# Performance work log

Measured on AMD Instinct MI355X. Metric: run time of the kernel, lower is better.

Reference implementation:

```python
import jax, jax.numpy as jnp
import numpy as np

N_NODES = 100000
N_EDGES = 1000000
IN_DIM = 128
OUT_DIM = 64


def setup_inputs() -> dict:
    key = jax.random.key(0)
    k1, k2, k3, k4, k5 = jax.random.split(key, 5)
    X = jax.random.normal(k1, (N_NODES, IN_DIM), dtype=jnp.float32)
    edge_rows = jax.random.randint(k2, (N_EDGES,), 0, N_NODES, dtype=jnp.int64)
    edge_cols = jax.random.randint(k3, (N_EDGES,), 0, N_NODES, dtype=jnp.int64)
    # normalized adjacency values (e.g. 1/sqrt(d_i d_j)), positive and small
    edge_vals = jax.random.uniform(k4, (N_EDGES,), dtype=jnp.float32, minval=0.0, maxval=1.0)
    # xavier-uniform-ish weight
    limit = float(np.sqrt(6.0 / (IN_DIM + OUT_DIM)))
    W = jax.random.uniform(k5, (IN_DIM, OUT_DIM), dtype=jnp.float32, minval=-limit, maxval=limit)
    bias = jnp.zeros((OUT_DIM,), dtype=jnp.float32)
    return {"X": X, "edge_rows": edge_rows, "edge_cols": edge_cols,
            "edge_vals": edge_vals, "W": W, "bias": bias}


def reference(X, edge_rows, edge_cols, edge_vals, W, bias):
    # dense projection: (N, in_dim) @ (in_dim, out_dim) -> (N, out_dim)
    h = X @ W
    # spmm over COO sparse A_norm: out[r] += v * h[c] for each edge (r, c, v)
    msg = edge_vals[:, None] * h[edge_cols]          # (E, out_dim) gather
    agg = jax.ops.segment_sum(msg, edge_rows, num_segments=N_NODES)
    return jax.nn.relu(agg + bias)
```

## Files before the change

### kernel.cpp

```cpp
#include <hip/hip_runtime.h>

#define IN_DIM 128
#define OUT_DIM 64
#define RPB_SHIFT 6
#define RPB 64
#define NBMAX 2048
#define CHUNK 4096
#define SLABCAP 896
#define PADK 136

typedef __attribute__((ext_vector_type(8))) short bf16x8;
typedef __attribute__((ext_vector_type(4))) float f32x4;
typedef __attribute__((ext_vector_type(4))) unsigned short us4;

__device__ inline unsigned short f2bf(float f) {
  unsigned u = __float_as_uint(f);
  u += 0x7FFFu + ((u >> 16) & 1u);
  return (unsigned short)(u >> 16);
}

__global__ __launch_bounds__(256) void zero_int_kernel(int* __restrict__ p, int n) {
  int i = blockIdx.x * 256 + threadIdx.x;
  for (; i < n; i += gridDim.x * 256) p[i] = 0;
}

__global__ __launch_bounds__(512) void fat_kernel(const float* __restrict__ X,
                                                  const float* __restrict__ W,
                                                  unsigned short* __restrict__ H,
                                                  const int* __restrict__ rows,
                                                  const int* __restrict__ cols,
                                                  const float* __restrict__ vals,
                                                  int* __restrict__ cursor,
                                                  uint2* __restrict__ staged,
                                                  int n, int ne, int nb, int nPart) {
  __shared__ __align__(16) unsigned char smem[34816];
  const int t = threadIdx.x;

  if ((int)blockIdx.x < nPart) {
    int* lh    = (int*)smem;
    int* lbase = (int*)(smem + NBMAX * 4);
    const int e0 = blockIdx.x * CHUNK;
    const int e1 = min(e0 + CHUNK, ne);

    for (int i = t; i < nb; i += 512) lh[i] = 0;
    __syncthreads();

    for (int i = e0 + t; i < e1; i += 512)
      atomicAdd(&lh[rows[i] >> RPB_SHIFT], 1);
    __syncthreads();

    for (int i = t; i < nb; i += 512) {
      int c = lh[i];
      lbase[i] = c ? atomicAdd(&cursor[i], c) : 0;
    }
    __syncthreads();
    for (int i = t; i < nb; i += 512) lh[i] = 0;
    __syncthreads();

    for (int i = e0 + t; i < e1; i += 512) {
      int r = rows[i];
      int b = r >> RPB_SHIFT;
      int lofs = atomicAdd(&lh[b], 1);
      int pos = lbase[b] + lofs;
      if (pos < SLABCAP) {
        unsigned key = ((unsigned)(r & (RPB - 1)) << 17) | (unsigned)cols[i];
        staged[(size_t)b * SLABCAP + pos] = make_uint2(key, __float_as_uint(vals[i]));
      }
    }
  } else {
    unsigned short (*Xs)[PADK] = (unsigned short(*)[PADK])smem;
    unsigned short (*Wt)[PADK] = (unsigned short(*)[PADK])(smem + 17408);
    const int lane = t & 63;
    const int wave = t >> 6;
    const int sub = wave & 3;
    const int ch = wave >> 2;
    const int row0 = ((int)blockIdx.x - nPart) * 64;

    {
      const float4* w4 = (const float4*)W;
#pragma unroll
      for (int j = 0; j < 4; ++j) {
        int i4 = t + j * 512;
        int k = i4 >> 4;
        int c = (i4 & 15) * 4;
        float4 v = w4[i4];
        Wt[c + 0][k] = f2bf(v.x);
        Wt[c + 1][k] = f2bf(v.y);
        Wt[c + 2][k] = f2bf(v.z);
        Wt[c + 3][k] = f2bf(v.w);
      }
    }
    {
#pragma unroll
      for (int j = 0; j < 4; ++j) {
        int i4 = t + j * 512;
        int r = i4 >> 5;
        int c4 = i4 & 31;
        int row = row0 + r;
        if (row < n) {
          float4 v = ((const float4*)(X + (size_t)row * IN_DIM))[c4];
          us4 p;
          p.x = f2bf(v.x); p.y = f2bf(v.y); p.z = f2bf(v.z); p.w = f2bf(v.w);
          *(us4*)&Xs[r][c4 * 4] = p;
        }
      }
    }
    __syncthreads();

    f32x4 acc[2] = {};
    const int arow = sub * 16 + (lane & 15);
    const int kg = (lane >> 4) * 8;
#pragma unroll
    for (int kk = 0; kk < 4; ++kk) {
      bf16x8 a = *(const bf16x8*)&Xs[arow][kk * 32 + kg];
#pragma unroll
      for (int nt = 0; nt < 2; ++nt) {
        bf16x8 b = *(const bf16x8*)&Wt[ch * 32 + nt * 16 + (lane & 15)][kk * 32 + kg];
        acc[nt] = __builtin_amdgcn_mfma_f32_16x16x32_bf16(a, b, acc[nt], 0, 0, 0);
      }
    }

    const int orow0 = row0 + sub * 16 + (lane >> 4) * 4;
#pragma unroll
    for (int nt = 0; nt < 2; ++nt) {
      int col = ch * 32 + nt * 16 + (lane & 15);
#pragma unroll
      for (int r = 0; r < 4; ++r) {
        int row = orow0 + r;
        if (row < n) H[(size_t)row * OUT_DIM + col] = f2bf(acc[nt][r]);
      }
    }
  }
}

__global__ __launch_bounds__(512) void spmm_fused_kernel(const int* __restrict__ cursor,
                                                         const uint2* __restrict__ staged,
                                                         const unsigned short* __restrict__ H,
                                                         const float* __restrict__ bias,
                                                         float* __restrict__ out, int n) {
  __shared__ uint2 sorted[SLABCAP];
  __shared__ int rcnt[RPB];
  __shared__ int rstart[RPB];
  __shared__ int rcur[RPB];

  const int b = blockIdx.x;
  const int t = threadIdx.x;
  const int cnt = min(cursor[b], SLABCAP);
  const uint2* slab = staged + (size_t)b * SLABCAP;

  if (t < RPB) rcnt[t] = 0;
  __syncthreads();
  for (int i = t; i < cnt; i += 512) atomicAdd(&rcnt[slab[i].x >> 17], 1);
  __syncthreads();

  if (t < RPB) {
    int v = rcnt[t];
    int x = v;
#pragma unroll
    for (int d = 1; d < RPB; d <<= 1) {
      int y = __shfl_up(x, d);
      if (t >= d) x += y;
    }
    rstart[t] = x - v;
    rcur[t] = x - v;
  }
  __syncthreads();

  for (int i = t; i < cnt; i += 512) {
    uint2 e = slab[i];
    int rl = e.x >> 17;
    int pos = atomicAdd(&rcur[rl], 1);
    sorted[pos] = e;
  }
  __syncthreads();

  const int lane = t & 63;
  const int wave = t >> 6;
  const int q4 = (lane & 15) * 4;
  const float4 bv = *(const float4*)&bias[q4];
  const int row0 = b << RPB_SHIFT;

  for (int rl = wave * 4 + ((lane >> 4) & 3); rl < RPB; rl += 32) {
    const int s = rstart[rl];
    const int c = rcnt[rl];
    float a0 = 0.f, a1 = 0.f, a2 = 0.f, a3 = 0.f;
    int e = 0;
    for (; e + 4 <= c; e += 4) {
      float v[4];
      uint2 hu[4];
#pragma unroll
      for (int k = 0; k < 4; ++k) {
        uint2 en = sorted[s + e + k];
        hu[k] = *(const uint2*)&H[(size_t)(en.x & 0x1FFFF) * OUT_DIM + q4];
        v[k] = __uint_as_float(en.y);
      }
#pragma unroll
      for (int k = 0; k < 4; ++k) {
        a0 = fmaf(v[k], __uint_as_float(hu[k].x << 16), a0);
        a1 = fmaf(v[k], __uint_as_float(hu[k].x & 0xFFFF0000u), a1);
        a2 = fmaf(v[k], __uint_as_float(hu[k].y << 16), a2);
        a3 = fmaf(v[k], __uint_as_float(hu[k].y & 0xFFFF0000u), a3);
      }
    }
    for (; e < c; ++e) {
      uint2 en = sorted[s + e];
      uint2 hu = *(const uint2*)&H[(size_t)(en.x & 0x1FFFF) * OUT_DIM + q4];
      float v = __uint_as_float(en.y);
      a0 = fmaf(v, __uint_as_float(hu.x << 16), a0);
      a1 = fmaf(v, __uint_as_float(hu.x & 0xFFFF0000u), a1);
      a2 = fmaf(v, __uint_as_float(hu.y << 16), a2);
      a3 = fmaf(v, __uint_as_float(hu.y & 0xFFFF0000u), a3);
    }
    int row = row0 + rl;
    if (row < n) {
      float4 o;
      o.x = fmaxf(a0 + bv.x, 0.f);
      o.y = fmaxf(a1 + bv.y, 0.f);
      o.z = fmaxf(a2 + bv.z, 0.f);
      o.w = fmaxf(a3 + bv.w, 0.f);
      *(float4*)(out + (size_t)row * OUT_DIM + q4) = o;
    }
  }
}

extern "C" void kernel_launch(void* const* d_in, const int* in_sizes, int n_in,
                              void* d_out, int out_size, void* d_ws, size_t ws_size,
                              hipStream_t stream) {
  const float* X    = (const float*)d_in[0];
  const int*   rows = (const int*)d_in[1];
  const int*   cols = (const int*)d_in[2];
  const float* vals = (const float*)d_in[3];
  const float* W    = (const float*)d_in[4];
  const float* bias = (const float*)d_in[5];
  float* out = (float*)d_out;

  const int n_nodes = in_sizes[0] / IN_DIM;
  const int n_edges = in_sizes[1];
  const int nb = (n_nodes + RPB - 1) >> RPB_SHIFT;

  char* ws = (char*)d_ws;
  unsigned short* H = (unsigned short*)ws;
  size_t off = (size_t)n_nodes * OUT_DIM * sizeof(unsigned short);
  off = (off + 15) & ~(size_t)15;
  int* cursor  = (int*)(ws + off); off += NBMAX * 4;
  uint2* staged = (uint2*)(ws + off);

  const int nPart = (n_edges + CHUNK - 1) / CHUNK;
  const int nGemm = (n_nodes + 63) / 64;

  zero_int_kernel<<<8, 256, 0, stream>>>(cursor, nb);
  fat_kernel<<<nPart + nGemm, 512, 0, stream>>>(X, W, H, rows, cols, vals, cursor, staged,
                                                n_nodes, n_edges, nb, nPart);
  spmm_fused_kernel<<<nb, 512, 0, stream>>>(cursor, staged, H, bias, out, n_nodes);
}
```

Measured before the change: 64.24 us.

## Split fused kernel into prep, GEMM, and sub-slab atomic scatter kernels

Replaces the combined partition/GEMM kernel with three kernels. A prep kernel zeroes the cursors and pre-transposes W to bf16. The GEMM kernel reads X directly from global memory, with no LDS staging, and computes all 64 columns per wave. Edge bucketing now uses direct global atomics on eight sub-slabs per row block, keyed by block index, instead of per-block LDS histograms. This removes the two-pass histogram and reduces atomic contention, but it adds launches, serializes the GEMM and the scatter, and spreads capacity across fixed-size sub-slabs that could overflow.

```diff
diff --git a/kernel.cpp b/kernel.cpp
--- a/kernel.cpp
+++ b/kernel.cpp
@@ -4,10 +4,8 @@
 #define OUT_DIM 64
 #define RPB_SHIFT 6
 #define RPB 64
-#define NBMAX 2048
-#define CHUNK 4096
+#define SUBCAP 176
 #define SLABCAP 896
-#define PADK 136
 
 typedef __attribute__((ext_vector_type(8))) short bf16x8;
 typedef __attribute__((ext_vector_type(4))) float f32x4;
@@ -19,116 +17,79 @@
   return (unsigned short)(u >> 16);
 }
 
-__global__ __launch_bounds__(256) void zero_int_kernel(int* __restrict__ p, int n) {
-  int i = blockIdx.x * 256 + threadIdx.x;
-  for (; i < n; i += gridDim.x * 256) p[i] = 0;
-}
-
-__global__ __launch_bounds__(512) void fat_kernel(const float* __restrict__ X,
-                                                  const float* __restrict__ W,
-                                                  unsigned short* __restrict__ H,
-                                                  const int* __restrict__ rows,
-                                                  const int* __restrict__ cols,
-                                                  const float* __restrict__ vals,
-                                                  int* __restrict__ cursor,
-                                                  uint2* __restrict__ staged,
-                                                  int n, int ne, int nb, int nPart) {
-  __shared__ __align__(16) unsigned char smem[34816];
+__global__ __launch_bounds__(256) void prep_kernel(const float* __restrict__ W,
+                                                   unsigned short* __restrict__ WT,
+                                                   int* __restrict__ cursor, int ncur) {
+  const int bid = blockIdx.x, t = threadIdx.x;
+  if (bid < 8) {
+    for (int i = bid * 256 + t; i < ncur; i += 8 * 256) cursor[i] = 0;
+  } else {
+    int gid = (bid - 8) * 256 + t;
+    int c = gid >> 5;
+    int kb = (gid & 31) * 4;
+    us4 p;
+    p.x = f2bf(W[(kb + 0) * OUT_DIM + c]);
+    p.y = f2bf(W[(kb + 1) * OUT_DIM + c]);
+    p.z = f2bf(W[(kb + 2) * OUT_DIM + c]);
+    p.w = f2bf(W[(kb + 3) * OUT_DIM + c]);
+    *(us4*)(WT + c * IN_DIM + kb) = p;
+  }
+}
+
+__global__ __launch_bounds__(256) void gemm_kernel(const float* __restrict__ X,
+                                                   const unsigned short* __restrict__ WT,
+                                                   unsigned short* __restrict__ H, int n) {
   const int t = threadIdx.x;
-
-  if ((int)blockIdx.x < nPart) {
-    int* lh    = (int*)smem;
-    int* lbase = (int*)(smem + NBMAX * 4);
-    const int e0 = blockIdx.x * CHUNK;
-    const int e1 = min(e0 + CHUNK, ne);
-
-    for (int i = t; i < nb; i += 512) lh[i] = 0;
-    __syncthreads();
-
-    for (int i = e0 + t; i < e1; i += 512)
-      atomicAdd(&lh[rows[i] >> RPB_SHIFT], 1);
-    __syncthreads();
-
-    for (int i = t; i < nb; i += 512) {
-      int c = lh[i];
-      lbase[i] = c ? atomicAdd(&cursor[i], c) : 0;
-    }
-    __syncthreads();
-    for (int i = t; i < nb; i += 512) lh[i] = 0;
-    __syncthreads();
-
-    for (int i = e0 + t; i < e1; i += 512) {
-      int r = rows[i];
-      int b = r >> RPB_SHIFT;
-      int lofs = atomicAdd(&lh[b], 1);
-      int pos = lbase[b] + lofs;
-      if (pos < SLABCAP) {
-        unsigned key = ((unsigned)(r & (RPB - 1)) << 17) | (unsigned)cols[i];
-        staged[(size_t)b * SLABCAP + pos] = make_uint2(key, __float_as_uint(vals[i]));
-      }
-    }
-  } else {
-    unsigned short (*Xs)[PADK] = (unsigned short(*)[PADK])smem;
-    unsigned short (*Wt)[PADK] = (unsigned short(*)[PADK])(smem + 17408);
-    const int lane = t & 63;
-    const int wave = t >> 6;
-    const int sub = wave & 3;
-    const int ch = wave >> 2;
-    const int row0 = ((int)blockIdx.x - nPart) * 64;
-
-    {
-      const float4* w4 = (const float4*)W;
-#pragma unroll
-      for (int j = 0; j < 4; ++j) {
-        int i4 = t + j * 512;
-        int k = i4 >> 4;
-        int c = (i4 & 15) * 4;
-        float4 v = w4[i4];
-        Wt[c + 0][k] = f2bf(v.x);
-        Wt[c + 1][k] = f2bf(v.y);
-        Wt[c + 2][k] = f2bf(v.z);
-        Wt[c + 3][k] = f2bf(v.w);
-      }
-    }
-    {
-#pragma unroll
-      for (int j = 0; j < 4; ++j) {
-        int i4 = t + j * 512;
-        int r = i4 >> 5;
-        int c4 = i4 & 31;
-        int row = row0 + r;
-        if (row < n) {
-          float4 v = ((const float4*)(X + (size_t)row * IN_DIM))[c4];
-          us4 p;
-          p.x = f2bf(v.x); p.y = f2bf(v.y); p.z = f2bf(v.z); p.w = f2bf(v.w);
-          *(us4*)&Xs[r][c4 * 4] = p;
-        }
-      }
-    }
-    __syncthreads();
-
-    f32x4 acc[2] = {};
-    const int arow = sub * 16 + (lane & 15);
-    const int kg = (lane >> 4) * 8;
-#pragma unroll
-    for (int kk = 0; kk < 4; ++kk) {
-      bf16x8 a = *(const bf16x8*)&Xs[arow][kk * 32 + kg];
-#pragma unroll
-      for (int nt = 0; nt < 2; ++nt) {
-        bf16x8 b = *(const bf16x8*)&Wt[ch * 32 + nt * 16 + (lane & 15)][kk * 32 + kg];
-        acc[nt] = __builtin_amdgcn_mfma_f32_16x16x32_bf16(a, b, acc[nt], 0, 0, 0);
-      }
-    }
-
-    const int orow0 = row0 + sub * 16 + (lane >> 4) * 4;
-#pragma unroll
-    for (int nt = 0; nt < 2; ++nt) {
-      int col = ch * 32 + nt * 16 + (lane & 15);
-#pragma unroll
-      for (int r = 0; r < 4; ++r) {
-        int row = orow0 + r;
-        if (row < n) H[(size_t)row * OUT_DIM + col] = f2bf(acc[nt][r]);
-      }
+  const int lane = t & 63;
+  const int sub = t >> 6;
+  const int row0 = blockIdx.x * 64;
+  const int r16 = lane & 15;
+  const int kg = (lane >> 4) * 8;
+  const int rowA = min(row0 + sub * 16 + r16, n - 1);
+  const float* xr = X + (size_t)rowA * IN_DIM + kg;
+
+  f32x4 acc[4] = {};
+#pragma unroll
+  for (int kk = 0; kk < 4; ++kk) {
+    float4 u = *(const float4*)(xr + kk * 32);
+    float4 v = *(const float4*)(xr + kk * 32 + 4);
+    bf16x8 a;
+    a[0] = (short)f2bf(u.x); a[1] = (short)f2bf(u.y);
+    a[2] = (short)f2bf(u.z); a[3] = (short)f2bf(u.w);
+    a[4] = (short)f2bf(v.x); a[5] = (short)f2bf(v.y);
+    a[6] = (short)f2bf(v.z); a[7] = (short)f2bf(v.w);
+#pragma unroll
+    for (int ct = 0; ct < 4; ++ct) {
+      bf16x8 b = *(const bf16x8*)(WT + (ct * 16 + r16) * IN_DIM + kk * 32 + kg);
+      acc[ct] = __builtin_amdgcn_mfma_f32_16x16x32_bf16(a, b, acc[ct], 0, 0, 0);
+    }
+  }
+
+  const int orow0 = row0 + sub * 16 + (lane >> 4) * 4;
+#pragma unroll
+  for (int ct = 0; ct < 4; ++ct) {
+    int col = ct * 16 + r16;
+#pragma unroll
+    for (int r = 0; r < 4; ++r) {
+      int row = orow0 + r;
+      if (row < n) H[(size_t)row * OUT_DIM + col] = f2bf(acc[ct][r]);
+    }
+  }
+}
+
+__global__ __launch_bounds__(256) void scatter_kernel(const int* __restrict__ rows,
+                                                      const int* __restrict__ cols,
+                                                      const float* __restrict__ vals,
+                                                      int* __restrict__ cursor,
+                                                      uint2* __restrict__ staged, int ne) {
+  const int g = blockIdx.x & 7;
+  for (int i = blockIdx.x * 256 + threadIdx.x; i < ne; i += gridDim.x * 256) {
+    int r = rows[i];
+    int slot = ((r >> RPB_SHIFT) << 3) + g;
+    int pos = atomicAdd(&cursor[slot], 1);
+    if (pos < SUBCAP) {
+      unsigned key = ((unsigned)(r & (RPB - 1)) << 17) | (unsigned)cols[i];
+      staged[(size_t)slot * SUBCAP + pos] = make_uint2(key, __float_as_uint(vals[i]));
     }
   }
 }
@@ -142,15 +103,32 @@
   __shared__ int rcnt[RPB];
   __shared__ int rstart[RPB];
   __shared__ int rcur[RPB];
+  __shared__ int segc[8];
 
   const int b = blockIdx.x;
   const int t = threadIdx.x;
-  const int cnt = min(cursor[b], SLABCAP);
-  const uint2* slab = staged + (size_t)b * SLABCAP;
-
+  const int lane = t & 63;
+  const int wave = t >> 6;
+
+  if (t < 8) segc[t] = min(cursor[b * 8 + t], SUBCAP);
   if (t < RPB) rcnt[t] = 0;
   __syncthreads();
-  for (int i = t; i < cnt; i += 512) atomicAdd(&rcnt[slab[i].x >> 17], 1);
+  if (t == 0) {
+    int s = 0;
+    for (int j = 0; j < 8; ++j) {
+      int c = segc[j];
+      if (s + c > SLABCAP) c = SLABCAP - s;
+      segc[j] = c;
+      s += c;
+    }
+  }
+  __syncthreads();
+
+  {
+    const uint2* seg = staged + (size_t)(b * 8 + wave) * SUBCAP;
+    const int c = segc[wave];
+    for (int i = lane; i < c; i += 64) atomicAdd(&rcnt[seg[i].x >> 17], 1);
+  }
   __syncthreads();
 
   if (t < RPB) {
@@ -166,16 +144,17 @@
   }
   __syncthreads();
 
-  for (int i = t; i < cnt; i += 512) {
-    uint2 e = slab[i];
-    int rl = e.x >> 17;
-    int pos = atomicAdd(&rcur[rl], 1);
-    sorted[pos] = e;
-  }
-  __syncthreads();
-
-  const int lane = t & 63;
-  const int wave = t >> 6;
+  {
+    const uint2* seg = staged + (size_t)(b * 8 + wave) * SUBCAP;
+    const int c = segc[wave];
+    for (int i = lane; i < c; i += 64) {
+      uint2 e = seg[i];
+      int pos = atomicAdd(&rcur[e.x >> 17], 1);
+      sorted[pos] = e;
+    }
+  }
+  __syncthreads();
+
   const int q4 = (lane & 15) * 4;
   const float4 bv = *(const float4*)&bias[q4];
   const int row0 = b << RPB_SHIFT;
@@ -241,15 +220,15 @@
   char* ws = (char*)d_ws;
   unsigned short* H = (unsigned short*)ws;
   size_t off = (size_t)n_nodes * OUT_DIM * sizeof(unsigned short);
-  off = (off + 15) & ~(size_t)15;
-  int* cursor  = (int*)(ws + off); off += NBMAX * 4;
+  off = (off + 255) & ~(size_t)255;
+  unsigned short* WT = (unsigned short*)(ws + off); off += OUT_DIM * IN_DIM * 2;
+  off = (off + 255) & ~(size_t)255;
+  int* cursor = (int*)(ws + off); off += (size_t)nb * 8 * 4;
+  off = (off + 255) & ~(size_t)255;
   uint2* staged = (uint2*)(ws + off);
 
-  const int nPart = (n_edges + CHUNK - 1) / CHUNK;
-  const int nGemm = (n_nodes + 63) / 64;
-
-  zero_int_kernel<<<8, 256, 0, stream>>>(cursor, nb);
-  fat_kernel<<<nPart + nGemm, 512, 0, stream>>>(X, W, H, rows, cols, vals, cursor, staged,
-                                                n_nodes, n_edges, nb, nPart);
+  prep_kernel<<<16, 256, 0, stream>>>(W, WT, cursor, nb * 8);
+  gemm_kernel<<<nb, 256, 0, stream>>>(X, WT, H, n_nodes);
+  scatter_kernel<<<2048, 256, 0, stream>>>(rows, cols, vals, cursor, staged, n_edges);
   spmm_fused_kernel<<<nb, 512, 0, stream>>>(cursor, staged, H, bias, out, n_nodes);
 }
```

Measured after the change: 113.9 us. 1.77x slower.

## Two-level bucket sort with coarse 512-row buckets and separate GEMM kernel

Applied to the files above, without the earlier changes.

Replaces the single-pass 64-row bucketing with a two-level scheme: a coarse kernel bins edges into 512-row buckets (one global atomic per bucket per chunk, far fewer than before), a split kernel sorts each coarse bucket by row into a global sorted array, and the SpMM kernel loads its 64-row window from that array. The GEMM is split out of the fused partition kernel into its own launch, and the coarse kernel keeps per-edge row and offset in registers instead of re-reading rows. This cuts global cursor atomics and scattered writes, but adds two kernel launches and an extra global round trip for staged edges. The serialized shared-memory scan with many barriers in the split kernel adds latency.

```diff
diff --git a/kernel.cpp b/kernel.cpp
--- a/kernel.cpp
+++ b/kernel.cpp
@@ -2,11 +2,13 @@
 
 #define IN_DIM 128
 #define OUT_DIM 64
-#define RPB_SHIFT 6
-#define RPB 64
-#define NBMAX 2048
+#define CB_SHIFT 9
+#define CB 512
+#define NBMAX 256
 #define CHUNK 4096
-#define SLABCAP 896
+#define EPT 8
+#define SLABCAP 5888
+#define SRTCAP 896
 #define PADK 136
 
 typedef __attribute__((ext_vector_type(8))) short bf16x8;
@@ -24,165 +26,195 @@
   for (; i < n; i += gridDim.x * 256) p[i] = 0;
 }
 
-__global__ __launch_bounds__(512) void fat_kernel(const float* __restrict__ X,
-                                                  const float* __restrict__ W,
-                                                  unsigned short* __restrict__ H,
-                                                  const int* __restrict__ rows,
-                                                  const int* __restrict__ cols,
-                                                  const float* __restrict__ vals,
-                                                  int* __restrict__ cursor,
-                                                  uint2* __restrict__ staged,
-                                                  int n, int ne, int nb, int nPart) {
-  __shared__ __align__(16) unsigned char smem[34816];
-  const int t = threadIdx.x;
-
-  if ((int)blockIdx.x < nPart) {
-    int* lh    = (int*)smem;
-    int* lbase = (int*)(smem + NBMAX * 4);
-    const int e0 = blockIdx.x * CHUNK;
-    const int e1 = min(e0 + CHUNK, ne);
-
-    for (int i = t; i < nb; i += 512) lh[i] = 0;
-    __syncthreads();
-
-    for (int i = e0 + t; i < e1; i += 512)
-      atomicAdd(&lh[rows[i] >> RPB_SHIFT], 1);
-    __syncthreads();
-
-    for (int i = t; i < nb; i += 512) {
-      int c = lh[i];
-      lbase[i] = c ? atomicAdd(&cursor[i], c) : 0;
-    }
-    __syncthreads();
-    for (int i = t; i < nb; i += 512) lh[i] = 0;
-    __syncthreads();
-
-    for (int i = e0 + t; i < e1; i += 512) {
+__global__ __launch_bounds__(256) void gemm_kernel(const float* __restrict__ X,
+                                                   const float* __restrict__ W,
+                                                   unsigned short* __restrict__ H, int n) {
+  __shared__ __align__(16) unsigned short Xs[64][PADK];
+  __shared__ __align__(16) unsigned short Wt[64][PADK];
+  const int t = threadIdx.x;
+  const int lane = t & 63;
+  const int wave = t >> 6;
+  const int row0 = blockIdx.x * 64;
+
+  {
+    const float4* w4 = (const float4*)W;
+#pragma unroll
+    for (int j = 0; j < 8; ++j) {
+      int i4 = t + j * 256;
+      int k = i4 >> 4;
+      int c = (i4 & 15) * 4;
+      float4 v = w4[i4];
+      Wt[c + 0][k] = f2bf(v.x);
+      Wt[c + 1][k] = f2bf(v.y);
+      Wt[c + 2][k] = f2bf(v.z);
+      Wt[c + 3][k] = f2bf(v.w);
+    }
+  }
+  {
+#pragma unroll
+    for (int j = 0; j < 8; ++j) {
+      int i4 = t + j * 256;
+      int r = i4 >> 5;
+      int c4 = i4 & 31;
+      int row = row0 + r;
+      if (row < n) {
+        float4 v = ((const float4*)(X + (size_t)row * IN_DIM))[c4];
+        us4 p;
+        p.x = f2bf(v.x); p.y = f2bf(v.y); p.z = f2bf(v.z); p.w = f2bf(v.w);
+        *(us4*)&Xs[r][c4 * 4] = p;
+      }
+    }
+  }
+  __syncthreads();
+
+  f32x4 acc[4] = {};
+  const int arow = wave * 16 + (lane & 15);
+  const int kg = (lane >> 4) * 8;
+#pragma unroll
+  for (int kk = 0; kk < 4; ++kk) {
+    bf16x8 a = *(const bf16x8*)&Xs[arow][kk * 32 + kg];
+#pragma unroll
+    for (int nt = 0; nt < 4; ++nt) {
+      bf16x8 b = *(const bf16x8*)&Wt[nt * 16 + (lane & 15)][kk * 32 + kg];
+      acc[nt] = __builtin_amdgcn_mfma_f32_16x16x32_bf16(a, b, acc[nt], 0, 0, 0);
+    }
+  }
+
+  const int orow0 = row0 + wave * 16 + (lane >> 4) * 4;
+#pragma unroll
+  for (int nt = 0; nt < 4; ++nt) {
+    int col = nt * 16 + (lane & 15);
+#pragma unroll
+    for (int r = 0; r < 4; ++r) {
+      int row = orow0 + r;
+      if (row < n) H[(size_t)row * OUT_DIM + col] = f2bf(acc[nt][r]);
+    }
+  }
+}
+
+__global__ __launch_bounds__(512) void coarse_kernel(const int* __restrict__ rows,
+                                                     const int* __restrict__ cols,
+                                                     const float* __restrict__ vals,
+                                                     int* __restrict__ cursor,
+                                                     uint2* __restrict__ staged,
+                                                     int ne, int nb) {
+  __shared__ int lh[NBMAX];
+  __shared__ int lbase[NBMAX];
+  const int t = threadIdx.x;
+  const int e0 = blockIdx.x * CHUNK;
+
+  if (t < NBMAX) lh[t] = 0;
+  __syncthreads();
+
+  int er[EPT], elofs[EPT];
+#pragma unroll
+  for (int k = 0; k < EPT; ++k) {
+    int i = e0 + t + k * 512;
+    if (i < ne) {
       int r = rows[i];
-      int b = r >> RPB_SHIFT;
-      int lofs = atomicAdd(&lh[b], 1);
-      int pos = lbase[b] + lofs;
+      er[k] = r;
+      elofs[k] = atomicAdd(&lh[r >> CB_SHIFT], 1);
+    } else {
+      er[k] = -1; elofs[k] = 0;
+    }
+  }
+  __syncthreads();
+
+  if (t < NBMAX) {
+    int c = (t < nb) ? lh[t] : 0;
+    lbase[t] = c ? atomicAdd(&cursor[t], c) : 0;
+  }
+  __syncthreads();
+
+#pragma unroll
+  for (int k = 0; k < EPT; ++k) {
+    int i = e0 + t + k * 512;
+    if (er[k] >= 0) {
+      int b = er[k] >> CB_SHIFT;
+      int pos = lbase[b] + elofs[k];
       if (pos < SLABCAP) {
-        unsigned key = ((unsigned)(r & (RPB - 1)) << 17) | (unsigned)cols[i];
+        unsigned key = ((unsigned)(er[k] & (CB - 1)) << 17) | (unsigned)cols[i];
         staged[(size_t)b * SLABCAP + pos] = make_uint2(key, __float_as_uint(vals[i]));
       }
     }
-  } else {
-    unsigned short (*Xs)[PADK] = (unsigned short(*)[PADK])smem;
-    unsigned short (*Wt)[PADK] = (unsigned short(*)[PADK])(smem + 17408);
-    const int lane = t & 63;
-    const int wave = t >> 6;
-    const int sub = wave & 3;
-    const int ch = wave >> 2;
-    const int row0 = ((int)blockIdx.x - nPart) * 64;
-
-    {
-      const float4* w4 = (const float4*)W;
-#pragma unroll
-      for (int j = 0; j < 4; ++j) {
-        int i4 = t + j * 512;
-        int k = i4 >> 4;
-        int c = (i4 & 15) * 4;
-        float4 v = w4[i4];
-        Wt[c + 0][k] = f2bf(v.x);
-        Wt[c + 1][k] = f2bf(v.y);
-        Wt[c + 2][k] = f2bf(v.z);
-        Wt[c + 3][k] = f2bf(v.w);
-      }
-    }
-    {
-#pragma unroll
-      for (int j = 0; j < 4; ++j) {
-        int i4 = t + j * 512;
-        int r = i4 >> 5;
-        int c4 = i4 & 31;
-        int row = row0 + r;
-        if (row < n) {
-          float4 v = ((const float4*)(X + (size_t)row * IN_DIM))[c4];
-          us4 p;
-          p.x = f2bf(v.x); p.y = f2bf(v.y); p.z = f2bf(v.z); p.w = f2bf(v.w);
-          *(us4*)&Xs[r][c4 * 4] = p;
-        }
-      }
-    }
-    __syncthreads();
-
-    f32x4 acc[2] = {};
-    const int arow = sub * 16 + (lane & 15);
-    const int kg = (lane >> 4) * 8;
-#pragma unroll
-    for (int kk = 0; kk < 4; ++kk) {
-      bf16x8 a = *(const bf16x8*)&Xs[arow][kk * 32 + kg];
-#pragma unroll
-      for (int nt = 0; nt < 2; ++nt) {
-        bf16x8 b = *(const bf16x8*)&Wt[ch * 32 + nt * 16 + (lane & 15)][kk * 32 + kg];
-        acc[nt] = __builtin_amdgcn_mfma_f32_16x16x32_bf16(a, b, acc[nt], 0, 0, 0);
-      }
-    }
-
-    const int orow0 = row0 + sub * 16 + (lane >> 4) * 4;
-#pragma unroll
-    for (int nt = 0; nt < 2; ++nt) {
-      int col = ch * 32 + nt * 16 + (lane & 15);
-#pragma unroll
-      for (int r = 0; r < 4; ++r) {
-        int row = orow0 + r;
-        if (row < n) H[(size_t)row * OUT_DIM + col] = f2bf(acc[nt][r]);
-      }
-    }
-  }
-}
-
-__global__ __launch_bounds__(512) void spmm_fused_kernel(const int* __restrict__ cursor,
-                                                         const uint2* __restrict__ staged,
-                                                         const unsigned short* __restrict__ H,
-                                                         const float* __restrict__ bias,
-                                                         float* __restrict__ out, int n) {
-  __shared__ uint2 sorted[SLABCAP];
-  __shared__ int rcnt[RPB];
-  __shared__ int rstart[RPB];
-  __shared__ int rcur[RPB];
+  }
+}
+
+__global__ __launch_bounds__(512) void split_kernel(const int* __restrict__ cursor,
+                                                    const uint2* __restrict__ staged,
+                                                    uint2* __restrict__ sorted_g,
+                                                    int* __restrict__ rowstart,
+                                                    int* __restrict__ rcntg) {
+  __shared__ int rcnt[CB];
+  __shared__ int sc[CB];
+  __shared__ int rcur[CB];
 
   const int b = blockIdx.x;
   const int t = threadIdx.x;
   const int cnt = min(cursor[b], SLABCAP);
   const uint2* slab = staged + (size_t)b * SLABCAP;
-
-  if (t < RPB) rcnt[t] = 0;
-  __syncthreads();
-  for (int i = t; i < cnt; i += 512) atomicAdd(&rcnt[slab[i].x >> 17], 1);
-  __syncthreads();
-
-  if (t < RPB) {
-    int v = rcnt[t];
-    int x = v;
-#pragma unroll
-    for (int d = 1; d < RPB; d <<= 1) {
-      int y = __shfl_up(x, d);
-      if (t >= d) x += y;
-    }
-    rstart[t] = x - v;
-    rcur[t] = x - v;
-  }
+  const int base = b * SLABCAP;
+
+  rcnt[t] = 0;
+  __syncthreads();
+  for (int i = t; i < cnt; i += 512) atomicAdd(&rcnt[(slab[i].x >> 17) & (CB - 1)], 1);
+  __syncthreads();
+
+  int v = rcnt[t];
+  sc[t] = v;
+  __syncthreads();
+#pragma unroll
+  for (int d = 1; d < CB; d <<= 1) {
+    int a = (t >= d) ? sc[t - d] : 0;
+    __syncthreads();
+    sc[t] += a;
+    __syncthreads();
+  }
+  const int excl = sc[t] - v;
+  rcur[t] = excl;
+  rowstart[b * CB + t] = base + excl;
+  rcntg[b * CB + t] = v;
   __syncthreads();
 
   for (int i = t; i < cnt; i += 512) {
     uint2 e = slab[i];
-    int rl = e.x >> 17;
-    int pos = atomicAdd(&rcur[rl], 1);
-    sorted[pos] = e;
-  }
+    int pos = atomicAdd(&rcur[(e.x >> 17) & (CB - 1)], 1);
+    sorted_g[base + pos] = e;
+  }
+}
+
+__global__ __launch_bounds__(512) void spmm_kernel(const uint2* __restrict__ sorted_g,
+                                                   const int* __restrict__ rowstart,
+                                                   const int* __restrict__ rcntg,
+                                                   const unsigned short* __restrict__ H,
+                                                   const float* __restrict__ bias,
+                                                   float* __restrict__ out, int n) {
+  __shared__ uint2 lent[SRTCAP];
+  __shared__ int rs[64];
+  __shared__ int rc[64];
+
+  const int t = threadIdx.x;
+  const int row0 = blockIdx.x * 64;
+
+  if (t < 64) {
+    rs[t] = rowstart[row0 + t];
+    rc[t] = rcntg[row0 + t];
+  }
+  __syncthreads();
+
+  const int base = rs[0];
+  const int len = min(rs[63] + rc[63] - base, SRTCAP);
+  for (int i = t; i < len; i += 512) lent[i] = sorted_g[base + i];
   __syncthreads();
 
   const int lane = t & 63;
   const int wave = t >> 6;
   const int q4 = (lane & 15) * 4;
   const float4 bv = *(const float4*)&bias[q4];
-  const int row0 = b << RPB_SHIFT;
-
-  for (int rl = wave * 4 + ((lane >> 4) & 3); rl < RPB; rl += 32) {
-    const int s = rstart[rl];
-    const int c = rcnt[rl];
+
+  for (int rl = wave * 4 + ((lane >> 4) & 3); rl < 64; rl += 32) {
+    const int s = rs[rl] - base;
+    const int c = min(rc[rl], SRTCAP - s);
     float a0 = 0.f, a1 = 0.f, a2 = 0.f, a3 = 0.f;
     int e = 0;
     for (; e + 4 <= c; e += 4) {
@@ -190,7 +222,7 @@
       uint2 hu[4];
 #pragma unroll
       for (int k = 0; k < 4; ++k) {
-        uint2 en = sorted[s + e + k];
+        uint2 en = lent[s + e + k];
         hu[k] = *(const uint2*)&H[(size_t)(en.x & 0x1FFFF) * OUT_DIM + q4];
         v[k] = __uint_as_float(en.y);
       }
@@ -203,7 +235,7 @@
       }
     }
     for (; e < c; ++e) {
-      uint2 en = sorted[s + e];
+      uint2 en = lent[s + e];
       uint2 hu = *(const uint2*)&H[(size_t)(en.x & 0x1FFFF) * OUT_DIM + q4];
       float v = __uint_as_float(en.y);
       a0 = fmaf(v, __uint_as_float(hu.x << 16), a0);
@@ -236,20 +268,26 @@
 
   const int n_nodes = in_sizes[0] / IN_DIM;
   const int n_edges = in_sizes[1];
-  const int nb = (n_nodes + RPB - 1) >> RPB_SHIFT;
+  const int nb = (n_nodes + CB - 1) >> CB_SHIFT;
 
   char* ws = (char*)d_ws;
   unsigned short* H = (unsigned short*)ws;
   size_t off = (size_t)n_nodes * OUT_DIM * sizeof(unsigned short);
-  off = (off + 15) & ~(size_t)15;
-  int* cursor  = (int*)(ws + off); off += NBMAX * 4;
-  uint2* staged = (uint2*)(ws + off);
+  off = (off + 255) & ~(size_t)255;
+  int* cursor = (int*)(ws + off); off += NBMAX * 4;
+  off = (off + 255) & ~(size_t)255;
+  int* rowstart = (int*)(ws + off); off += (size_t)nb * CB * 4;
+  int* rcntg    = (int*)(ws + off); off += (size_t)nb * CB * 4;
+  off = (off + 255) & ~(size_t)255;
+  uint2* staged   = (uint2*)(ws + off); off += (size_t)nb * SLABCAP * 8;
+  uint2* sorted_g = (uint2*)(ws + off);
 
   const int nPart = (n_edges + CHUNK - 1) / CHUNK;
   const int nGemm = (n_nodes + 63) / 64;
 
-  zero_int_kernel<<<8, 256, 0, stream>>>(cursor, nb);
-  fat_kernel<<<nPart + nGemm, 512, 0, stream>>>(X, W, H, rows, cols, vals, cursor, staged,
-                                                n_nodes, n_edges, nb, nPart);
-  spmm_fused_kernel<<<nb, 512, 0, stream>>>(cursor, staged, H, bias, out, n_nodes);
-}
+  zero_int_kernel<<<1, 256, 0, stream>>>(cursor, nb);
+  gemm_kernel<<<nGemm, 256, 0, stream>>>(X, W, H, n_nodes);
+  coarse_kernel<<<nPart, 512, 0, stream>>>(rows, cols, vals, cursor, staged, n_edges, nb);
+  split_kernel<<<nb, 512, 0, stream>>>(cursor, staged, sorted_g, rowstart, rcntg);
+  spmm_kernel<<<nGemm, 512, 0, stream>>>(sorted_g, rowstart, rcntg, H, bias, out, n_nodes);
+}
```

Measured after the change: 73.90 us. 15.0% more time.

## Split fused GEMM/partition kernel into separate GEMM and register-cached partition kernels

Applied to the files above, without the earlier changes.

Replaces the heterogeneous fat kernel, where blocks either ran the bf16 MFMA projection or the edge bucketing, with two separate launches. The GEMM kernel now uses 256 threads, with each wave covering all 64 output columns. The partition kernel uses 1024 threads and keeps each edge's row and local offset in registers, so rows are read once and the second histogram pass is gone. This removes the divergent block roles and the extra reads and barriers, but adds a kernel launch and loses the overlap between the GEMM and partition work.

```diff
diff --git a/kernel.cpp b/kernel.cpp
--- a/kernel.cpp
+++ b/kernel.cpp
@@ -6,6 +6,7 @@
 #define RPB 64
 #define NBMAX 2048
 #define CHUNK 4096
+#define EPT 4
 #define SLABCAP 896
 #define PADK 136
 
@@ -24,110 +25,115 @@
   for (; i < n; i += gridDim.x * 256) p[i] = 0;
 }
 
-__global__ __launch_bounds__(512) void fat_kernel(const float* __restrict__ X,
-                                                  const float* __restrict__ W,
-                                                  unsigned short* __restrict__ H,
-                                                  const int* __restrict__ rows,
-                                                  const int* __restrict__ cols,
-                                                  const float* __restrict__ vals,
-                                                  int* __restrict__ cursor,
-                                                  uint2* __restrict__ staged,
-                                                  int n, int ne, int nb, int nPart) {
-  __shared__ __align__(16) unsigned char smem[34816];
+__global__ __launch_bounds__(256) void gemm_kernel(const float* __restrict__ X,
+                                                   const float* __restrict__ W,
+                                                   unsigned short* __restrict__ H, int n) {
+  __shared__ __align__(16) unsigned short Xs[64][PADK];
+  __shared__ __align__(16) unsigned short Wt[64][PADK];
   const int t = threadIdx.x;
-
-  if ((int)blockIdx.x < nPart) {
-    int* lh    = (int*)smem;
-    int* lbase = (int*)(smem + NBMAX * 4);
-    const int e0 = blockIdx.x * CHUNK;
-    const int e1 = min(e0 + CHUNK, ne);
-
-    for (int i = t; i < nb; i += 512) lh[i] = 0;
-    __syncthreads();
-
-    for (int i = e0 + t; i < e1; i += 512)
-      atomicAdd(&lh[rows[i] >> RPB_SHIFT], 1);
-    __syncthreads();
-
-    for (int i = t; i < nb; i += 512) {
-      int c = lh[i];
-      lbase[i] = c ? atomicAdd(&cursor[i], c) : 0;
-    }
-    __syncthreads();
-    for (int i = t; i < nb; i += 512) lh[i] = 0;
-    __syncthreads();
-
-    for (int i = e0 + t; i < e1; i += 512) {
+  const int lane = t & 63;
+  const int wave = t >> 6;
+  const int row0 = blockIdx.x * 64;
+
+  {
+    const float4* w4 = (const float4*)W;
+#pragma unroll
+    for (int j = 0; j < 8; ++j) {
+      int i4 = t + j * 256;
+      int k = i4 >> 4;
+      int c = (i4 & 15) * 4;
+      float4 v = w4[i4];
+      Wt[c + 0][k] = f2bf(v.x);
+      Wt[c + 1][k] = f2bf(v.y);
+      Wt[c + 2][k] = f2bf(v.z);
+      Wt[c + 3][k] = f2bf(v.w);
+    }
+  }
+  {
+#pragma unroll
+    for (int j = 0; j < 8; ++j) {
+      int i4 = t + j * 256;
+      int r = i4 >> 5;
+      int c4 = i4 & 31;
+      int row = row0 + r;
+      if (row < n) {
+        float4 v = ((const float4*)(X + (size_t)row * IN_DIM))[c4];
+        us4 p;
+        p.x = f2bf(v.x); p.y = f2bf(v.y); p.z = f2bf(v.z); p.w = f2bf(v.w);
+        *(us4*)&Xs[r][c4 * 4] = p;
+      }
+    }
+  }
+  __syncthreads();
+
+  f32x4 acc[4] = {};
+  const int arow = wave * 16 + (lane & 15);
+  const int kg = (lane >> 4) * 8;
+#pragma unroll
+  for (int kk = 0; kk < 4; ++kk) {
+    bf16x8 a = *(const bf16x8*)&Xs[arow][kk * 32 + kg];
+#pragma unroll
+    for (int nt = 0; nt < 4; ++nt) {
+      bf16x8 b = *(const bf16x8*)&Wt[nt * 16 + (lane & 15)][kk * 32 + kg];
+      acc[nt] = __builtin_amdgcn_mfma_f32_16x16x32_bf16(a, b, acc[nt], 0, 0, 0);
+    }
+  }
+
+  const int orow0 = row0 + wave * 16 + (lane >> 4) * 4;
+#pragma unroll
+  for (int nt = 0; nt < 4; ++nt) {
+    int col = nt * 16 + (lane & 15);
+#pragma unroll
+    for (int r = 0; r < 4; ++r) {
+      int row = orow0 + r;
+      if (row < n) H[(size_t)row * OUT_DIM + col] = f2bf(acc[nt][r]);
+    }
+  }
+}
+
+__global__ __launch_bounds__(1024) void partition_kernel(const int* __restrict__ rows,
+                                                         const int* __restrict__ cols,
+                                                         const float* __restrict__ vals,
+                                                         int* __restrict__ cursor,
+                                                         uint2* __restrict__ staged,
+                                                         int ne, int nb) {
+  __shared__ int lh[NBMAX];
+  __shared__ int lbase[NBMAX];
+  const int t = threadIdx.x;
+  const int e0 = blockIdx.x * CHUNK;
+
+  for (int i = t; i < nb; i += 1024) lh[i] = 0;
+  __syncthreads();
+
+  int er[EPT], elofs[EPT];
+#pragma unroll
+  for (int k = 0; k < EPT; ++k) {
+    int i = e0 + t + k * 1024;
+    if (i < ne) {
       int r = rows[i];
-      int b = r >> RPB_SHIFT;
-      int lofs = atomicAdd(&lh[b], 1);
-      int pos = lbase[b] + lofs;
+      er[k] = r;
+      elofs[k] = atomicAdd(&lh[r >> RPB_SHIFT], 1);
+    } else {
+      er[k] = -1; elofs[k] = 0;
+    }
+  }
+  __syncthreads();
+
+  for (int i = t; i < nb; i += 1024) {
+    int c = lh[i];
+    lbase[i] = c ? atomicAdd(&cursor[i], c) : 0;
+  }
+  __syncthreads();
+
+#pragma unroll
+  for (int k = 0; k < EPT; ++k) {
+    int i = e0 + t + k * 1024;
+    if (er[k] >= 0) {
+      int b = er[k] >> RPB_SHIFT;
+      int pos = lbase[b] + elofs[k];
       if (pos < SLABCAP) {
-        unsigned key = ((unsigned)(r & (RPB - 1)) << 17) | (unsigned)cols[i];
+        unsigned key = ((unsigned)(er[k] & (RPB - 1)) << 17) | (unsigned)cols[i];
         staged[(size_t)b * SLABCAP + pos] = make_uint2(key, __float_as_uint(vals[i]));
-      }
-    }
-  } else {
-    unsigned short (*Xs)[PADK] = (unsigned short(*)[PADK])smem;
-    unsigned short (*Wt)[PADK] = (unsigned short(*)[PADK])(smem + 17408);
-    const int lane = t & 63;
-    const int wave = t >> 6;
-    const int sub = wave & 3;
-    const int ch = wave >> 2;
-    const int row0 = ((int)blockIdx.x - nPart) * 64;
-
-    {
-      const float4* w4 = (const float4*)W;
-#pragma unroll
-      for (int j = 0; j < 4; ++j) {
-        int i4 = t + j * 512;
-        int k = i4 >> 4;
-        int c = (i4 & 15) * 4;
-        float4 v = w4[i4];
-        Wt[c + 0][k] = f2bf(v.x);
-        Wt[c + 1][k] = f2bf(v.y);
-        Wt[c + 2][k] = f2bf(v.z);
-        Wt[c + 3][k] = f2bf(v.w);
-      }
-    }
-    {
-#pragma unroll
-      for (int j = 0; j < 4; ++j) {
-        int i4 = t + j * 512;
-        int r = i4 >> 5;
-        int c4 = i4 & 31;
-        int row = row0 + r;
-        if (row < n) {
-          float4 v = ((const float4*)(X + (size_t)row * IN_DIM))[c4];
-          us4 p;
-          p.x = f2bf(v.x); p.y = f2bf(v.y); p.z = f2bf(v.z); p.w = f2bf(v.w);
-          *(us4*)&Xs[r][c4 * 4] = p;
-        }
-      }
-    }
-    __syncthreads();
-
-    f32x4 acc[2] = {};
-    const int arow = sub * 16 + (lane & 15);
-    const int kg = (lane >> 4) * 8;
-#pragma unroll
-    for (int kk = 0; kk < 4; ++kk) {
-      bf16x8 a = *(const bf16x8*)&Xs[arow][kk * 32 + kg];
-#pragma unroll
-      for (int nt = 0; nt < 2; ++nt) {
-        bf16x8 b = *(const bf16x8*)&Wt[ch * 32 + nt * 16 + (lane & 15)][kk * 32 + kg];
-        acc[nt] = __builtin_amdgcn_mfma_f32_16x16x32_bf16(a, b, acc[nt], 0, 0, 0);
-      }
-    }
-
-    const int orow0 = row0 + sub * 16 + (lane >> 4) * 4;
-#pragma unroll
-    for (int nt = 0; nt < 2; ++nt) {
-      int col = ch * 32 + nt * 16 + (lane & 15);
-#pragma unroll
-      for (int r = 0; r < 4; ++r) {
-        int row = orow0 + r;
-        if (row < n) H[(size_t)row * OUT_DIM + col] = f2bf(acc[nt][r]);
       }
     }
   }
@@ -241,15 +247,16 @@
   char* ws = (char*)d_ws;
   unsigned short* H = (unsigned short*)ws;
   size_t off = (size_t)n_nodes * OUT_DIM * sizeof(unsigned short);
-  off = (off + 15) & ~(size_t)15;
-  int* cursor  = (int*)(ws + off); off += NBMAX * 4;
+  off = (off + 255) & ~(size_t)255;
+  int* cursor = (int*)(ws + off); off += (size_t)NBMAX * 4;
+  off = (off + 255) & ~(size_t)255;
   uint2* staged = (uint2*)(ws + off);
 
   const int nPart = (n_edges + CHUNK - 1) / CHUNK;
   const int nGemm = (n_nodes + 63) / 64;
 
-  zero_int_kernel<<<8, 256, 0, stream>>>(cursor, nb);
-  fat_kernel<<<nPart + nGemm, 512, 0, stream>>>(X, W, H, rows, cols, vals, cursor, staged,
-                                                n_nodes, n_edges, nb, nPart);
+  zero_int_kernel<<<4, 256, 0, stream>>>(cursor, nb);
+  gemm_kernel<<<nGemm, 256, 0, stream>>>(X, W, H, n_nodes);
+  partition_kernel<<<nPart, 1024, 0, stream>>>(rows, cols, vals, cursor, staged, n_edges, nb);
   spmm_fused_kernel<<<nb, 512, 0, stream>>>(cursor, staged, H, bias, out, n_nodes);
 }
```

Result: slower. 69.70 us (+8.5%).
